# Performance work log

Hardware: AMD Instinct MI355X
Metric: run time of the kernel (lower is better)

The kernel has to match this reference:

```python
import jax, jax.numpy as jnp
import numpy as np
import math

B, H, N, L = 8, 512, 64, 4096

def setup_inputs() -> dict:
    key = jax.random.key(0)
    k = jax.random.split(key, 8)
    u = jax.random.normal(k[0], (B, H, L), dtype=jnp.float32)
    log_dt = jax.random.uniform(k[1], (H,), dtype=jnp.float32) * (math.log(0.1) - math.log(0.001)) + math.log(0.001)
    C_re = jax.random.normal(k[2], (H, N // 2), dtype=jnp.float32)
    C_im = jax.random.normal(k[3], (H, N // 2), dtype=jnp.float32)
    log_A_real = jnp.log(0.5 * jnp.ones((H, N // 2), dtype=jnp.float32))
    A_imag = math.pi * jnp.broadcast_to(jnp.arange(N // 2, dtype=jnp.float32), (H, N // 2))
    D = jax.random.normal(k[4], (H,), dtype=jnp.float32)
    # 1x1 conv H -> 2H (weights stored (2H, H)), PyTorch-like init scale 1/sqrt(H)
    s = 1.0 / math.sqrt(H)
    W = jax.random.uniform(k[5], (2 * H, H), dtype=jnp.float32, minval=-s, maxval=s)
    b = jax.random.uniform(k[6], (2 * H,), dtype=jnp.float32, minval=-s, maxval=s)
    return {"u": u, "log_dt": log_dt, "C_re": C_re, "C_im": C_im,
            "log_A_real": log_A_real, "A_imag": A_imag, "D": D, "W": W, "b": b}

def reference(u, log_dt, C_re, C_im, log_A_real, A_imag, D, W, b):
    Lq = u.shape[-1]
    dt = jnp.exp(log_dt)                       # (H,)
    C = C_re + 1j * C_im                       # (H, N/2)
    A = -jnp.exp(log_A_real) + 1j * A_imag     # (H, N/2)
    dtA = A * dt[:, None]                      # (H, N/2)
    # Vandermonde: exp(dtA * l) for l in [0, L)
    Kv = jnp.exp(dtA[:, :, None] * jnp.arange(Lq, dtype=jnp.float32))  # (H, N/2, L)
    Ck = C * (jnp.exp(dtA) - 1.0) / A          # (H, N/2)
    k = 2.0 * jnp.einsum('hn,hnl->hl', Ck, Kv).real  # (H, L)
    # FFT-based causal convolution with length-2L zero padding
    k_f = jnp.fft.rfft(k, n=2 * Lq)            # (H, L+1)
    u_f = jnp.fft.rfft(u, n=2 * Lq)            # (B, H, L+1)
    y = jnp.fft.irfft(u_f * k_f, n=2 * Lq)[..., :Lq]  # (B, H, L)
    y = y + u * D[:, None]
    y = jax.nn.gelu(y, approximate=False)      # nn.GELU default (erf)
    # 1x1 conv H -> 2H then GLU over channel dim (-2)
    z = jnp.einsum('oh,bhl->bol', W, y) + b[:, None]   # (B, 2H, L)
    a, g = jnp.split(z, 2, axis=-2)
    return a * jax.nn.sigmoid(g)               # (B, H, L)
```

## Files before the change

### kernel.cpp

```cpp
#include <hip/hip_runtime.h>
#include <hip/hip_bf16.h>
#include <math.h>

#define Bb 8
#define Hh 512
#define N2 32
#define Ll 4096
#define CH 256
#define NCH 16

#define KG_OFF  8388608
#define CKR_OFF (KG_OFF + 131072)
#define CKI_OFF (CKR_OFF + 16384)
#define W256R_OFF (CKI_OFF + 16384)
#define W256I_OFF (W256R_OFF + 16384)
#define WNHI_OFF 18874368u
#define WNLO_OFF 27525120u

typedef short bf16x8 __attribute__((ext_vector_type(8)));
typedef float f32x4  __attribute__((ext_vector_type(4)));

__device__ __forceinline__ float gelu_f(float x) {
    return 0.5f * x * (1.f + erff(x * 0.70710678118654752f));
}
__device__ __forceinline__ unsigned short f2bf(float f) {
    __hip_bfloat16 h = __float2bfloat16(f);
    return *reinterpret_cast<unsigned short*>(&h);
}
__device__ __forceinline__ float bf2f(unsigned short s) {
    return __uint_as_float(((unsigned int)s) << 16);
}
__device__ __forceinline__ void gl2lds16(const void* g, void* l) {
    __builtin_amdgcn_global_load_lds(
        (const __attribute__((address_space(1))) void*)g,
        (__attribute__((address_space(3))) void*)l, 16, 0, 0);
}

__global__ __launch_bounds__(256) void s4d_k1(
    const float* __restrict__ log_dt,
    const float* __restrict__ C_re,  const float* __restrict__ C_im,
    const float* __restrict__ log_A_real, const float* __restrict__ A_imag,
    const float* __restrict__ W,
    float* __restrict__ scratch, unsigned short* __restrict__ Wb,
    unsigned short* __restrict__ wnhi, unsigned short* __restrict__ wnlo,
    unsigned short* __restrict__ wnt)
{
    __shared__ __align__(16) float wLr[N2][257];
    __shared__ __align__(16) float wLi[N2][257];
    __shared__ float Ck2r[N2], Ck2i[N2];

    const int tid = threadIdx.x;
    const int h = blockIdx.x;

    {
        const int i4 = (blockIdx.x * 256 + tid) * 4;
        const float4 wv = *(const float4*)&W[i4];
        unsigned short o[4] = {f2bf(wv.x), f2bf(wv.y), f2bf(wv.z), f2bf(wv.w)};
        *(uint2*)&Wb[i4] = *(uint2*)o;
    }

    const float dt = expf(log_dt[h]);
    const int n = tid & 31, tq = tid >> 5;

    const float lar = log_A_real[h * N2 + n];
    const float Aim = A_imag[h * N2 + n];
    const float Are = -expf(lar);
    const float dar = Are * dt, dai = Aim * dt;

    float wr, wi;
    { float e = expf(dar); float sn, cs; sincosf(dai, &sn, &cs); wr = e * cs; wi = e * sn; }
    const float j0 = (float)(32 * tq + 1);
    float cr, ci;
    { float e = expf(dar * j0); float sn, cs; sincosf(dai * j0, &sn, &cs); cr = e * cs; ci = e * sn; }
    #pragma unroll 8
    for (int i = 0; i < 32; ++i) {
        const int j = 32 * tq + i;
        wLr[n][j] = cr; wLi[n][j] = ci;
        const float tr = cr * wr - ci * wi;
        ci = cr * wi + ci * wr; cr = tr;
    }

    if (tid < N2) {
        const float er = wr - 1.f, ei = wi;
        const float den = Are * Are + Aim * Aim;
        const float qr = (er * Are + ei * Aim) / den;
        const float qi = (ei * Are - er * Aim) / den;
        const float c_r = C_re[h * N2 + tid], c_i = C_im[h * N2 + tid];
        const float k2r = 2.f * (c_r * qr - c_i * qi);
        const float k2i = 2.f * (c_r * qi + c_i * qr);
        Ck2r[tid] = k2r; Ck2i[tid] = k2i;
        scratch[CKR_OFF + h * 32 + tid] = k2r;
        scratch[CKI_OFF + h * 32 + tid] = k2i;
    }
    __syncthreads();

    {
        const int t = tid;
        float kv = 0.f;
        if (t == 0) {
            #pragma unroll
            for (int m = 0; m < N2; ++m) kv += Ck2r[m];
        } else {
            #pragma unroll
            for (int m = 0; m < N2; ++m)
                kv += Ck2r[m] * wLr[m][t - 1] - Ck2i[m] * wLi[m][t - 1];
        }
        scratch[KG_OFF + h * CH + t] = kv;
    }

    {
        unsigned short* WH  = wnhi + (size_t)h * (64 * 264);
        unsigned short* WLo = wnlo + (size_t)h * (64 * 136);
        unsigned short* WT  = wnt  + (size_t)h * (257 * 64);

        for (int idx = tid; idx < 64 * 33; idx += 256) {
            const int r = idx / 33, g = idx - 33 * r;
            const float* src = (r & 1) ? wLi[r >> 1] : wLr[r >> 1];
            __align__(16) unsigned short o[8];
            #pragma unroll
            for (int jj = 0; jj < 8; ++jj) {
                const int j = 8 * g + jj;
                const float v = (j == 0) ? ((r & 1) ? 0.f : 1.f)
                              : (j <= 256 ? src[j - 1] : 0.f);
                o[jj] = f2bf(v);
            }
            *(uint4*)&WH[r * 264 + 8 * g] = *(const uint4*)o;
        }
        for (int idx = tid; idx < 64 * 17; idx += 256) {
            const int r = idx / 17, g = idx - 17 * r;
            const float* src = (r & 1) ? wLi[r >> 1] : wLr[r >> 1];
            __align__(16) unsigned short o[8];
            #pragma unroll
            for (int jj = 0; jj < 8; ++jj) {
                const int j = 8 * g + jj;
                const float v = (j == 0) ? ((r & 1) ? 0.f : 1.f)
                              : (j < 128 ? src[j - 1] : 0.f);
                o[jj] = f2bf(v - bf2f(f2bf(v)));
            }
            *(uint4*)&WLo[r * 136 + 8 * g] = *(const uint4*)o;
        }
        for (int idx = tid; idx < 257 * 8; idx += 256) {
            const int t = idx >> 3, g = idx & 7;
            __align__(16) unsigned short o[8];
            #pragma unroll
            for (int rr = 0; rr < 8; ++rr) {
                const int r = 8 * g + rr;
                const float v = (t == 0) ? ((r & 1) ? 0.f : 1.f)
                              : ((r & 1) ? wLi[r >> 1][t - 1] : wLr[r >> 1][t - 1]);
                o[rr] = f2bf(v);
            }
            *(uint4*)&WT[t * 64 + 8 * g] = *(const uint4*)o;
        }
        if (tid < N2) {
            scratch[W256R_OFF + h * 32 + tid] = wLr[tid][255];
            scratch[W256I_OFF + h * 32 + tid] = wLi[tid][255];
        }
    }
}

__global__ __launch_bounds__(256, 3) void s4d_k23(
    const float* __restrict__ u,
    const float* __restrict__ Dp,
    const float* scratch,
    const unsigned short* wnhi, const unsigned short* wnlo,
    const unsigned short* wnt,
    unsigned short* y_bf)
{
    __shared__ __align__(16) unsigned short uhi[16 * 264];
    __shared__ __align__(16) unsigned short ulo[16 * 264];
    __shared__ __align__(16) unsigned short khi[8 * 520];
    __shared__ __align__(16) unsigned short klo[8 * 520];
    __shared__ __align__(16) float Plds[64 * 20];
    __shared__ __align__(16) unsigned short CkAhi[16 * 72];
    __shared__ __align__(16) unsigned short CkAlo[16 * 72];

    const int tid = threadIdx.x;
    const int x = blockIdx.x;
    const int h = ((x >> 6) << 3) | (x & 7);
    const int b = (x >> 3) & 7;
    const int wv = tid >> 6;
    const int lane = tid & 63;
    const int l15 = lane & 15;
    const int quad = lane >> 4;

    {
        unsigned int* z1 = (unsigned int*)khi;
        unsigned int* z2 = (unsigned int*)klo;
        for (int i = tid; i < 2080; i += 256) { z1[i] = 0; z2[i] = 0; }
    }
    const float* ub = u + (size_t)(b * Hh + h) * Ll;
    #pragma unroll
    for (int q = 0; q < 4; ++q) {
        const int l = q * 1024 + tid * 4;
        const float4 v = *(const float4*)&ub[l];
        const int c = l >> 8, s = l & 255;
        const unsigned short h3 = f2bf(v.w), h2 = f2bf(v.z), h1 = f2bf(v.y), h0 = f2bf(v.x);
        uint2 dh;
        dh.x = (unsigned int)h3 | ((unsigned int)h2 << 16);
        dh.y = (unsigned int)h1 | ((unsigned int)h0 << 16);
        *(uint2*)&uhi[c * 264 + (252 - s)] = dh;
        uint2 dl;
        dl.x = (unsigned int)f2bf(v.w - bf2f(h3)) | ((unsigned int)f2bf(v.z - bf2f(h2)) << 16);
        dl.y = (unsigned int)f2bf(v.y - bf2f(h1)) | ((unsigned int)f2bf(v.x - bf2f(h0)) << 16);
        *(uint2*)&ulo[c * 264 + (252 - s)] = dl;
    }
    const float kval = scratch[KG_OFF + h * CH + tid];
    const unsigned short k_hi = f2bf(kval);
    const unsigned short k_lo = f2bf(kval - bf2f(k_hi));
    __syncthreads();

    #pragma unroll
    for (int r = 0; r < 8; ++r) {
        const int x2 = tid + 255 - r;
        khi[r * 520 + x2] = k_hi;
        klo[r * 520 + x2] = k_lo;
    }
    {
        const unsigned short* WH = wnhi + (size_t)h * (64 * 264);
        const unsigned short* WL = wnlo + (size_t)h * (64 * 136);
        f32x4 accP = {0.f, 0.f, 0.f, 0.f};
        const int wrow = 16 * wv + l15;
        #pragma unroll
        for (int j0 = 0; j0 < 256; j0 += 32) {
            const bf16x8 ah = *(const bf16x8*)&uhi[l15 * 264 + j0 + 8 * quad];
            const bf16x8 al = *(const bf16x8*)&ulo[l15 * 264 + j0 + 8 * quad];
            const bf16x8 wh = *(const bf16x8*)&WH[wrow * 264 + j0 + 8 * quad];
            accP = __builtin_amdgcn_mfma_f32_16x16x32_bf16(ah, wh, accP, 0, 0, 0);
            accP = __builtin_amdgcn_mfma_f32_16x16x32_bf16(al, wh, accP, 0, 0, 0);
            if (j0 < 128) {
                const bf16x8 wl = *(const bf16x8*)&WL[wrow * 136 + j0 + 8 * quad];
                accP = __builtin_amdgcn_mfma_f32_16x16x32_bf16(ah, wl, accP, 0, 0, 0);
            }
        }
        *(f32x4*)&Plds[wrow * 20 + 4 * quad] = accP;
    }
    __syncthreads();

    bf16x8 sf[8];
    {
        const unsigned short* WT = wnt + (size_t)h * (257 * 64);
        #pragma unroll
        for (int ks2 = 0; ks2 < 2; ++ks2)
            #pragma unroll
            for (int i = 0; i < 4; ++i) {
                const int tcol = 16 * (wv + 4 * i) + l15 + 1;
                sf[ks2 * 4 + i] = *(const bf16x8*)&WT[tcol * 64 + 32 * ks2 + 8 * quad];
            }
    }

    if (tid < 32) {
        const int n = tid;
        const float k2r = scratch[CKR_OFF + h * 32 + n];
        const float k2i = scratch[CKI_OFF + h * 32 + n];
        const float wCr = scratch[W256R_OFF + h * 32 + n];
        const float wCi = scratch[W256I_OFF + h * 32 + n];
        float sr = 0.f, si = 0.f;
        #pragma unroll
        for (int c = 0; c < NCH; ++c) {
            const float vr = k2r * sr - k2i * si;
            const float vi = -(k2r * si + k2i * sr);
            const unsigned short vrh = f2bf(vr), vih = f2bf(vi);
            *(unsigned int*)&CkAhi[c * 72 + 2 * n] =
                (unsigned int)vrh | ((unsigned int)vih << 16);
            *(unsigned int*)&CkAlo[c * 72 + 2 * n] =
                (unsigned int)f2bf(vr - bf2f(vrh)) |
                ((unsigned int)f2bf(vi - bf2f(vih)) << 16);
            const float pr = Plds[(2 * n) * 20 + c], pi = Plds[(2 * n + 1) * 20 + c];
            const float nr = wCr * sr - wCi * si + pr;
            si = wCr * si + wCi * sr + pi;
            sr = nr;
        }
    }

    f32x4 acc[4];
    #pragma unroll
    for (int i = 0; i < 4; ++i) acc[i] = (f32x4){0.f, 0.f, 0.f, 0.f};
    {
        const int r = lane & 7;
        const int roff = r * 520;
        const int half = ((lane >> 3) & 1) * 8;
        #pragma unroll
        for (int i = 0; i < 4; ++i) {
            const int nt = wv + 4 * i;
            const int jstart = (240 - 16 * nt) & ~31;
            for (int j0 = jstart; j0 < 256; j0 += 32) {
                const bf16x8 ah = *(const bf16x8*)&uhi[l15 * 264 + j0 + 8 * quad];
                const bf16x8 al = *(const bf16x8*)&ulo[l15 * 264 + j0 + 8 * quad];
                const int base = 16 * nt + j0 + 8 * quad + half;
                const bf16x8 bh = *(const bf16x8*)&khi[roff + base];
                const bf16x8 bl = *(const bf16x8*)&klo[roff + base];
                acc[i] = __builtin_amdgcn_mfma_f32_16x16x32_bf16(ah, bh, acc[i], 0, 0, 0);
                acc[i] = __builtin_amdgcn_mfma_f32_16x16x32_bf16(ah, bl, acc[i], 0, 0, 0);
                acc[i] = __builtin_amdgcn_mfma_f32_16x16x32_bf16(al, bh, acc[i], 0, 0, 0);
            }
        }
    }
    __syncthreads();

    #pragma unroll
    for (int ks2 = 0; ks2 < 2; ++ks2) {
        const int ks = 32 * ks2;
        const bf16x8 ah = *(const bf16x8*)&CkAhi[l15 * 72 + ks + 8 * quad];
        const bf16x8 al = *(const bf16x8*)&CkAlo[l15 * 72 + ks + 8 * quad];
        #pragma unroll
        for (int i = 0; i < 4; ++i) {
            acc[i] = __builtin_amdgcn_mfma_f32_16x16x32_bf16(ah, sf[ks2 * 4 + i], acc[i], 0, 0, 0);
            acc[i] = __builtin_amdgcn_mfma_f32_16x16x32_bf16(al, sf[ks2 * 4 + i], acc[i], 0, 0, 0);
        }
    }

    const float Dh = Dp[h];
    unsigned short* yo = y_bf + (size_t)(b * Hh + h) * Ll;
    #pragma unroll
    for (int i = 0; i < 4; ++i) {
        const int t = 16 * (wv + 4 * i) + l15;
        const int jrev = 255 - t;
        #pragma unroll
        for (int rr = 0; rr < 4; ++rr) {
            const int c = 4 * quad + rr;
            const float uu = bf2f(uhi[c * 264 + jrev]) + bf2f(ulo[c * 264 + jrev]);
            const float yv = acc[i][rr] + Dh * uu;
            yo[c * 256 + t] = f2bf(gelu_f(yv));
        }
    }
}

__global__ __launch_bounds__(256) void s4d_T(
    const unsigned short* y_bf, unsigned short* __restrict__ y_T)
{
    __shared__ unsigned short T[64][72];
    const int tid = threadIdx.x;
    const int b  = blockIdx.x >> 9;
    const int k0 = ((blockIdx.x >> 6) & 7) << 6;
    const int l0 = (blockIdx.x & 63) << 6;

    #pragma unroll
    for (int q = 0; q < 2; ++q) {
        const int idx = tid + 256 * q;
        const int kk = idx >> 3, lg = idx & 7;
        const uint4 v = *(const uint4*)&y_bf[((size_t)(b * Hh + k0 + kk)) * Ll + l0 + 8 * lg];
        const int gp = lg ^ ((kk >> 3) & 7);
        *(uint4*)&T[kk][8 * gp] = v;
    }
    __syncthreads();
    #pragma unroll
    for (int q = 0; q < 2; ++q) {
        const int idx = tid + 256 * q;
        const int ll = idx >> 3, kg = idx & 7;
        unsigned short o[8];
        #pragma unroll
        for (int j = 0; j < 8; ++j) {
            const int kr = 8 * kg + j;
            const int gp = (ll >> 3) ^ kg;
            o[j] = T[kr][8 * gp + (ll & 7)];
        }
        *(uint4*)&y_T[((size_t)(b * Ll + l0 + ll)) * Hh + k0 + 8 * kg] = *(uint4*)o;
    }
}

__global__ __launch_bounds__(256, 4) void s4d_s2(
    const unsigned short* __restrict__ yT,
    const unsigned short* __restrict__ Wb,
    const float* __restrict__ bias,
    float* __restrict__ out)
{
    __shared__ __align__(16) unsigned short Wlds[128 * 64];
    __shared__ __align__(16) unsigned short Ylds[128 * 64];

    const int tid = threadIdx.x;
    const int ct = blockIdx.x;
    const int mt = blockIdx.y;
    const int b  = ct >> 5;
    const int l0 = (ct & 31) << 7;
    const int m0 = mt << 6;

    const int wv = tid >> 6, lane = tid & 63;
    const int l15 = lane & 15, quad = lane >> 4;

    f32x4 accA[8], accG[8];
    #pragma unroll
    for (int j = 0; j < 8; ++j) {
        accA[j] = (f32x4){0.f, 0.f, 0.f, 0.f};
        accG[j] = (f32x4){0.f, 0.f, 0.f, 0.f};
    }

    for (int kk = 0; kk < Hh; kk += 64) {
        #pragma unroll
        for (int q = 0; q < 4; ++q) {
            const int idx = tid + 256 * q;
            const int rr = idx >> 3, kg = idx & 7;
            const int sw = kg ^ (rr & 7);
            const int grow = m0 + rr + ((rr >> 6) * 448);
            gl2lds16(&Wb[grow * Hh + kk + 8 * sw], &Wlds[8 * idx]);
            gl2lds16(&yT[((size_t)(b * Ll + l0 + rr)) * Hh + kk + 8 * sw], &Ylds[8 * idx]);
        }
        __syncthreads();

        #pragma unroll
        for (int ks = 0; ks < 64; ks += 32) {
            const int c0 = (ks >> 3) + quad;
            const int arow = 16 * wv + l15;
            const bf16x8 af = *(const bf16x8*)&Wlds[arow * 64 + 8 * (c0 ^ (arow & 7))];
            const int grow2 = 64 + arow;
            const bf16x8 gf = *(const bf16x8*)&Wlds[grow2 * 64 + 8 * (c0 ^ (grow2 & 7))];
            #pragma unroll
            for (int j = 0; j < 8; ++j) {
                const int brow = 16 * j + l15;
                const bf16x8 bfr = *(const bf16x8*)&Ylds[brow * 64 + 8 * (c0 ^ (brow & 7))];
                accA[j] = __builtin_amdgcn_mfma_f32_16x16x32_bf16(af, bfr, accA[j], 0, 0, 0);
                accG[j] = __builtin_amdgcn_mfma_f32_16x16x32_bf16(gf, bfr, accG[j], 0, 0, 0);
            }
        }
        __syncthreads();
    }

    const int mb = m0 + 16 * wv + 4 * quad;
    float bA[4], bG[4];
    #pragma unroll
    for (int rr = 0; rr < 4; ++rr) { bA[rr] = bias[mb + rr]; bG[rr] = bias[mb + rr + 512]; }

    #pragma unroll
    for (int j = 0; j < 8; ++j) {
        const int l = l0 + 16 * j + l15;
        #pragma unroll
        for (int rr = 0; rr < 4; ++rr) {
            const float a = accA[j][rr] + bA[rr];
            const float g = accG[j][rr] + bG[rr];
            out[((size_t)(b * Hh + mb + rr)) * Ll + l] = a / (1.f + expf(-g));
        }
    }
}

extern "C" void kernel_launch(void* const* d_in, const int* in_sizes, int n_in,
                              void* d_out, int out_size, void* d_ws, size_t ws_size,
                              hipStream_t stream)
{
    const float* u          = (const float*)d_in[0];
    const float* log_dt     = (const float*)d_in[1];
    const float* C_re       = (const float*)d_in[2];
    const float* C_im       = (const float*)d_in[3];
    const float* log_A_real = (const float*)d_in[4];
    const float* A_imag     = (const float*)d_in[5];
    const float* Dp         = (const float*)d_in[6];
    const float* W          = (const float*)d_in[7];
    const float* bias       = (const float*)d_in[8];

    float* out = (float*)d_out;
    float* scratch = (float*)d_out;
    unsigned short* y_bf = (unsigned short*)d_out;
    unsigned short* wnhi = (unsigned short*)d_out + WNHI_OFF;
    unsigned short* wnlo = (unsigned short*)d_out + WNLO_OFF;
    unsigned short* y_T  = (unsigned short*)d_ws;
    unsigned short* wnt  = (unsigned short*)d_ws;
    unsigned short* Wb   = (unsigned short*)((char*)d_ws + (32u << 20));

    s4d_k1<<<dim3(Hh), dim3(256), 0, stream>>>(
        log_dt, C_re, C_im, log_A_real, A_imag, W, scratch, Wb, wnhi, wnlo, wnt);
    s4d_k23<<<dim3(Bb * Hh), dim3(256), 0, stream>>>(
        u, Dp, scratch, wnhi, wnlo, wnt, y_bf);
    s4d_T<<<dim3(Bb * Hh), dim3(256), 0, stream>>>(y_bf, y_T);
    s4d_s2<<<dim3(256, 8), dim3(256), 0, stream>>>(y_T, Wb, bias, out);
}
```

Measured before the change: 242.3 us.

## Load GEMM weights directly from global, remap grid, pad Plds stride, hoist scratch loads

In the final GEMM kernel, the weight tile no longer goes through LDS. Each wave reads its A and G weight fragments straight from global memory, which halves LDS use and the async copies per k-step. The 2D grid is flattened and remapped so blocks sharing the same y tile are neighbours, improving L2 reuse. In k23, the Plds stride changes from 20 to 17 to reduce bank conflicts, and the per-head scratch coefficients are loaded early so their latency overlaps other work. The trade-offs are scalar LDS stores and global-memory latency on the weight reads.

```diff
diff --git a/kernel.cpp b/kernel.cpp
--- a/kernel.cpp
+++ b/kernel.cpp
@@ -170,7 +170,7 @@
     __shared__ __align__(16) unsigned short ulo[16 * 264];
     __shared__ __align__(16) unsigned short khi[8 * 520];
     __shared__ __align__(16) unsigned short klo[8 * 520];
-    __shared__ __align__(16) float Plds[64 * 20];
+    __shared__ __align__(16) float Plds[64 * 17];
     __shared__ __align__(16) unsigned short CkAhi[16 * 72];
     __shared__ __align__(16) unsigned short CkAlo[16 * 72];
 
@@ -182,6 +182,12 @@
     const int lane = tid & 63;
     const int l15 = lane & 15;
     const int quad = lane >> 4;
+
+    const int nsc = tid & 31;
+    const float sc_k2r = scratch[CKR_OFF + h * 32 + nsc];
+    const float sc_k2i = scratch[CKI_OFF + h * 32 + nsc];
+    const float sc_wCr = scratch[W256R_OFF + h * 32 + nsc];
+    const float sc_wCi = scratch[W256I_OFF + h * 32 + nsc];
 
     {
         unsigned int* z1 = (unsigned int*)khi;
@@ -232,7 +238,11 @@
                 accP = __builtin_amdgcn_mfma_f32_16x16x32_bf16(ah, wl, accP, 0, 0, 0);
             }
         }
-        *(f32x4*)&Plds[wrow * 20 + 4 * quad] = accP;
+        const int pbase = wrow * 17 + 4 * quad;
+        Plds[pbase + 0] = accP[0];
+        Plds[pbase + 1] = accP[1];
+        Plds[pbase + 2] = accP[2];
+        Plds[pbase + 3] = accP[3];
     }
     __syncthreads();
 
@@ -250,10 +260,8 @@
 
     if (tid < 32) {
         const int n = tid;
-        const float k2r = scratch[CKR_OFF + h * 32 + n];
-        const float k2i = scratch[CKI_OFF + h * 32 + n];
-        const float wCr = scratch[W256R_OFF + h * 32 + n];
-        const float wCi = scratch[W256I_OFF + h * 32 + n];
+        const float k2r = sc_k2r, k2i = sc_k2i;
+        const float wCr = sc_wCr, wCi = sc_wCi;
         float sr = 0.f, si = 0.f;
         #pragma unroll
         for (int c = 0; c < NCH; ++c) {
@@ -265,7 +273,7 @@
             *(unsigned int*)&CkAlo[c * 72 + 2 * n] =
                 (unsigned int)f2bf(vr - bf2f(vrh)) |
                 ((unsigned int)f2bf(vi - bf2f(vih)) << 16);
-            const float pr = Plds[(2 * n) * 20 + c], pi = Plds[(2 * n + 1) * 20 + c];
+            const float pr = Plds[(2 * n) * 17 + c], pi = Plds[(2 * n + 1) * 17 + c];
             const float nr = wCr * sr - wCi * si + pr;
             si = wCr * si + wCi * sr + pi;
             sr = nr;
@@ -364,14 +372,14 @@
     const float* __restrict__ bias,
     float* __restrict__ out)
 {
-    __shared__ __align__(16) unsigned short Wlds[128 * 64];
     __shared__ __align__(16) unsigned short Ylds[128 * 64];
 
     const int tid = threadIdx.x;
-    const int ct = blockIdx.x;
-    const int mt = blockIdx.y;
-    const int b  = ct >> 5;
-    const int l0 = (ct & 31) << 7;
+    const int x  = blockIdx.x;
+    const int ctg = ((x >> 6) << 3) | (x & 7);
+    const int mt  = (x >> 3) & 7;
+    const int b  = ctg >> 5;
+    const int l0 = (ctg & 31) << 7;
     const int m0 = mt << 6;
 
     const int wv = tid >> 6, lane = tid & 63;
@@ -383,6 +391,9 @@
         accA[j] = (f32x4){0.f, 0.f, 0.f, 0.f};
         accG[j] = (f32x4){0.f, 0.f, 0.f, 0.f};
     }
+
+    const unsigned short* Wa = Wb + (size_t)(m0 + 16 * wv + l15) * Hh;
+    const unsigned short* Wg = Wb + (size_t)(512 + m0 + 16 * wv + l15) * Hh;
 
     for (int kk = 0; kk < Hh; kk += 64) {
         #pragma unroll
@@ -390,8 +401,6 @@
             const int idx = tid + 256 * q;
             const int rr = idx >> 3, kg = idx & 7;
             const int sw = kg ^ (rr & 7);
-            const int grow = m0 + rr + ((rr >> 6) * 448);
-            gl2lds16(&Wb[grow * Hh + kk + 8 * sw], &Wlds[8 * idx]);
             gl2lds16(&yT[((size_t)(b * Ll + l0 + rr)) * Hh + kk + 8 * sw], &Ylds[8 * idx]);
         }
         __syncthreads();
@@ -399,10 +408,8 @@
         #pragma unroll
         for (int ks = 0; ks < 64; ks += 32) {
             const int c0 = (ks >> 3) + quad;
-            const int arow = 16 * wv + l15;
-            const bf16x8 af = *(const bf16x8*)&Wlds[arow * 64 + 8 * (c0 ^ (arow & 7))];
-            const int grow2 = 64 + arow;
-            const bf16x8 gf = *(const bf16x8*)&Wlds[grow2 * 64 + 8 * (c0 ^ (grow2 & 7))];
+            const bf16x8 af = *(const bf16x8*)&Wa[kk + 8 * c0];
+            const bf16x8 gf = *(const bf16x8*)&Wg[kk + 8 * c0];
             #pragma unroll
             for (int j = 0; j < 8; ++j) {
                 const int brow = 16 * j + l15;
@@ -459,5 +466,5 @@
     s4d_k23<<<dim3(Bb * Hh), dim3(256), 0, stream>>>(
         u, Dp, scratch, wnhi, wnlo, wnt, y_bf);
     s4d_T<<<dim3(Bb * Hh), dim3(256), 0, stream>>>(y_bf, y_T);
-    s4d_s2<<<dim3(256, 8), dim3(256), 0, stream>>>(y_T, Wb, bias, out);
-}
+    s4d_s2<<<dim3(2048), dim3(256), 0, stream>>>(y_T, Wb, bias, out);
+}
```

Result: no change. 243.5 us (+0.5%).
